# Optimization experiments

Hardware: AMD Instinct MI355X
Metric: run time of the kernel (lower is better)

## Reference

```python
import jax, jax.numpy as jnp
import numpy as np

HIDDEN = 128
N_NODES = 50000
N_NEI = 32


def setup_inputs() -> dict:
    key = jax.random.key(0)
    k1, k2, k3, k4, k5, k6 = jax.random.split(key, 6)
    x = jax.random.normal(k1, (N_NODES, HIDDEN), dtype=jnp.float32)
    neibour = jax.random.normal(k2, (N_NODES, N_NEI, HIDDEN), dtype=jnp.float32)
    sub_graph = jax.random.normal(k3, (N_NODES, HIDDEN), dtype=jnp.float32)
    pmi = jax.random.normal(k4, (N_NODES, N_NEI), dtype=jnp.float32)
    nei_pad_mask = jnp.zeros((N_NODES, N_NEI), dtype=jnp.float32)
    # nn.Linear(2H, 1): store weight as [2H, 1] plus bias [1]
    bound = 1.0 / np.sqrt(2 * HIDDEN)
    W = jax.random.uniform(k5, (2 * HIDDEN, 1), jnp.float32, -bound, bound)
    b = jax.random.uniform(k6, (1,), jnp.float32, -bound, bound)
    return {"x": x, "neibour": neibour, "sub_graph": sub_graph,
            "pmi": pmi, "nei_pad_mask": nei_pad_mask, "W": W, "b": b}


def reference(x, neibour, sub_graph, pmi, nei_pad_mask, W, b):
    # torch: cat([neibour, expand(sub_graph)], -1) @ W + b  (Linear(2H,1))
    # Split W so we never materialize the [N,K,2H] concat: same math.
    H = sub_graph.shape[-1]
    Wn, Ws = W[:H], W[H:]                                   # [H,1] each
    s = (jnp.einsum('nkh,ho->nko', neibour, Wn)             # [N,K,1]
         + jnp.einsum('nh,ho->no', sub_graph, Ws)[:, None, :]
         + b)
    score = jax.nn.sigmoid(s).sum(-1)                       # sum over singleton out dim -> [N,K]
    score = score + nei_pad_mask
    return jax.nn.softmax(score, axis=-1)
```

## Files before the change

### kernel.cpp

```cpp
#include <hip/hip_runtime.h>
#include <hip/hip_bf16.h>

#define HIDDEN 128
#define N_NEI 32

__device__ __forceinline__ float merge2(float a, float b, int m, int lane) {
    const bool hi = (lane & m) != 0;
    const float keep = hi ? b : a;
    const float send = hi ? a : b;
    return keep + __shfl_xor(send, m, 64);
}

__global__ __launch_bounds__(256) void score_softmax_kernel(
    const float* __restrict__ neibour,
    const float* __restrict__ sub_graph,
    const float* __restrict__ nei_pad_mask,
    const float* __restrict__ W,
    const float* __restrict__ b,
    float* __restrict__ out,
    int n_nodes)
{
    const int wave = threadIdx.x >> 6;
    const int lane = threadIdx.x & 63;
    const int node = blockIdx.x * 4 + wave;
    if (node >= n_nodes) return;

    const int half = lane >> 5;
    const int l32  = lane & 31;

    const float4 wn = *reinterpret_cast<const float4*>(W + l32 * 4);

    const float2 sg = *reinterpret_cast<const float2*>(sub_graph + (size_t)node * HIDDEN + lane * 2);
    const float2 ws = *reinterpret_cast<const float2*>(W + HIDDEN + lane * 2);
    float sn = fmaf(sg.x, ws.x, sg.y * ws.y);
    #pragma unroll
    for (int m = 1; m < 64; m <<= 1) sn += __shfl_xor(sn, m, 64);
    sn += b[0];

    const float* nb = neibour + (size_t)node * (N_NEI * HIDDEN);
    float p[16];
    #pragma unroll
    for (int kk = 0; kk < 16; ++kk) {
        const float4 v = *reinterpret_cast<const float4*>(nb + (2 * kk + half) * HIDDEN + l32 * 4);
        p[kk] = fmaf(v.x, wn.x, fmaf(v.y, wn.y, fmaf(v.z, wn.z, v.w * wn.w)));
    }

    float r[8];
    #pragma unroll
    for (int i = 0; i < 8; ++i) r[i] = merge2(p[2*i], p[2*i+1], 16, lane);
    float s4[4];
    #pragma unroll
    for (int i = 0; i < 4; ++i) s4[i] = merge2(r[2*i], r[2*i+1], 8, lane);
    float t2[2];
    #pragma unroll
    for (int i = 0; i < 2; ++i) t2[i] = merge2(s4[2*i], s4[2*i+1], 4, lane);
    float u = merge2(t2[0], t2[1], 2, lane);
    u += __shfl_xor(u, 1, 64);

    const int pidx = ((lane >> 4) & 1) | (((lane >> 3) & 1) << 1)
                   | (((lane >> 2) & 1) << 2) | (((lane >> 1) & 1) << 3);
    const int row = 2 * pidx + half;

    float sc = u + sn;
    sc = 1.0f / (1.0f + __expf(-sc));
    sc += nei_pad_mask[(size_t)node * N_NEI + row];

    float mx = sc;
    #pragma unroll
    for (int m = 1; m < 64; m <<= 1) mx = fmaxf(mx, __shfl_xor(mx, m, 64));
    float e = __expf(sc - mx);
    float ssum = e;
    #pragma unroll
    for (int m = 1; m < 64; m <<= 1) ssum += __shfl_xor(ssum, m, 64);

    if ((lane & 1) == 0)
        out[(size_t)node * N_NEI + row] = e * 2.0f / ssum;
}

extern "C" void kernel_launch(void* const* d_in, const int* in_sizes, int n_in,
                              void* d_out, int out_size, void* d_ws, size_t ws_size,
                              hipStream_t stream) {
    const float* neibour      = (const float*)d_in[1];
    const float* sub_graph    = (const float*)d_in[2];
    const float* nei_pad_mask = (const float*)d_in[4];
    const float* W            = (const float*)d_in[5];
    const float* b            = (const float*)d_in[6];
    float* out = (float*)d_out;

    const int n_nodes = in_sizes[4] / N_NEI;
    const int blocks  = (n_nodes + 3) / 4;

    score_softmax_kernel<<<blocks, 256, 0, stream>>>(
        neibour, sub_graph, nei_pad_mask, W, b, out, n_nodes);
}
```

Baseline: 148.9 us.

## Use persistent grid-stride waves with register prefetch of the next node

Launches a fixed grid of 1024 blocks in which each wave loops over nodes with a grid stride. The next node's neighbour rows, sub_graph slice and mask are loaded into registers before the current node's reductions and softmax run, so memory latency overlaps with compute. Loads and stores use nontemporal hints, and the max/sum reductions skip the redundant xor-1 step because lane pairs already hold duplicate values. The cost is roughly double the vector register use for the prefetch buffer, which may cut occupancy, and fewer waves in flight overall.

```diff
diff --git a/kernel.cpp b/kernel.cpp
--- a/kernel.cpp
+++ b/kernel.cpp
@@ -3,6 +3,8 @@
 
 #define HIDDEN 128
 #define N_NEI 32
+
+typedef float f32x4 __attribute__((ext_vector_type(4)));
 
 __device__ __forceinline__ float merge2(float a, float b, int m, int lane) {
     const bool hi = (lane & m) != 0;
@@ -22,59 +24,87 @@
 {
     const int wave = threadIdx.x >> 6;
     const int lane = threadIdx.x & 63;
-    const int node = blockIdx.x * 4 + wave;
-    if (node >= n_nodes) return;
-
     const int half = lane >> 5;
     const int l32  = lane & 31;
-
-    const float4 wn = *reinterpret_cast<const float4*>(W + l32 * 4);
-
-    const float2 sg = *reinterpret_cast<const float2*>(sub_graph + (size_t)node * HIDDEN + lane * 2);
-    const float2 ws = *reinterpret_cast<const float2*>(W + HIDDEN + lane * 2);
-    float sn = fmaf(sg.x, ws.x, sg.y * ws.y);
-    #pragma unroll
-    for (int m = 1; m < 64; m <<= 1) sn += __shfl_xor(sn, m, 64);
-    sn += b[0];
-
-    const float* nb = neibour + (size_t)node * (N_NEI * HIDDEN);
-    float p[16];
-    #pragma unroll
-    for (int kk = 0; kk < 16; ++kk) {
-        const float4 v = *reinterpret_cast<const float4*>(nb + (2 * kk + half) * HIDDEN + l32 * 4);
-        p[kk] = fmaf(v.x, wn.x, fmaf(v.y, wn.y, fmaf(v.z, wn.z, v.w * wn.w)));
-    }
-
-    float r[8];
-    #pragma unroll
-    for (int i = 0; i < 8; ++i) r[i] = merge2(p[2*i], p[2*i+1], 16, lane);
-    float s4[4];
-    #pragma unroll
-    for (int i = 0; i < 4; ++i) s4[i] = merge2(r[2*i], r[2*i+1], 8, lane);
-    float t2[2];
-    #pragma unroll
-    for (int i = 0; i < 2; ++i) t2[i] = merge2(s4[2*i], s4[2*i+1], 4, lane);
-    float u = merge2(t2[0], t2[1], 2, lane);
-    u += __shfl_xor(u, 1, 64);
+    const int wgid = blockIdx.x * 4 + wave;
+    const int wstride = gridDim.x * 4;
 
     const int pidx = ((lane >> 4) & 1) | (((lane >> 3) & 1) << 1)
                    | (((lane >> 2) & 1) << 2) | (((lane >> 1) & 1) << 3);
     const int row = 2 * pidx + half;
 
-    float sc = u + sn;
-    sc = 1.0f / (1.0f + __expf(-sc));
-    sc += nei_pad_mask[(size_t)node * N_NEI + row];
+    const f32x4 wn = *reinterpret_cast<const f32x4*>(W + l32 * 4);
+    const float2 ws = *reinterpret_cast<const float2*>(W + HIDDEN + lane * 2);
+    const float bias = b[0];
 
-    float mx = sc;
-    #pragma unroll
-    for (int m = 1; m < 64; m <<= 1) mx = fmaxf(mx, __shfl_xor(mx, m, 64));
-    float e = __expf(sc - mx);
-    float ssum = e;
-    #pragma unroll
-    for (int m = 1; m < 64; m <<= 1) ssum += __shfl_xor(ssum, m, 64);
+    int node = wgid;
+    if (node >= n_nodes) return;
 
-    if ((lane & 1) == 0)
-        out[(size_t)node * N_NEI + row] = e * 2.0f / ssum;
+    f32x4 v[16];
+    float2 sgv;
+    float maskv;
+
+#define LOAD_NODE(nd) do {                                                    \
+        const float* nb_ = neibour + (size_t)(nd) * (N_NEI * HIDDEN);         \
+        _Pragma("unroll")                                                     \
+        for (int kk = 0; kk < 16; ++kk)                                       \
+            v[kk] = __builtin_nontemporal_load(                               \
+                reinterpret_cast<const f32x4*>(nb_ + (2 * kk + half) * HIDDEN \
+                                               + l32 * 4));                   \
+        sgv = *reinterpret_cast<const float2*>(                               \
+            sub_graph + (size_t)(nd) * HIDDEN + lane * 2);                    \
+        maskv = nei_pad_mask[(size_t)(nd) * N_NEI + row];                     \
+    } while (0)
+
+    LOAD_NODE(node);
+
+    #pragma unroll 1
+    while (node < n_nodes) {
+        float p[16];
+        #pragma unroll
+        for (int kk = 0; kk < 16; ++kk)
+            p[kk] = fmaf(v[kk].x, wn.x, fmaf(v[kk].y, wn.y,
+                     fmaf(v[kk].z, wn.z, v[kk].w * wn.w)));
+        float sn = fmaf(sgv.x, ws.x, sgv.y * ws.y);
+        const float mask_cur = maskv;
+
+        const int next = node + wstride;
+        if (next < n_nodes) LOAD_NODE(next);
+
+        #pragma unroll
+        for (int m = 1; m < 64; m <<= 1) sn += __shfl_xor(sn, m, 64);
+        sn += bias;
+
+        float r[8];
+        #pragma unroll
+        for (int i = 0; i < 8; ++i) r[i] = merge2(p[2*i], p[2*i+1], 16, lane);
+        float s4[4];
+        #pragma unroll
+        for (int i = 0; i < 4; ++i) s4[i] = merge2(r[2*i], r[2*i+1], 8, lane);
+        float t2[2];
+        #pragma unroll
+        for (int i = 0; i < 2; ++i) t2[i] = merge2(s4[2*i], s4[2*i+1], 4, lane);
+        float u = merge2(t2[0], t2[1], 2, lane);
+        u += __shfl_xor(u, 1, 64);
+
+        float sc = u + sn;
+        sc = 1.0f / (1.0f + __expf(-sc));
+        sc += mask_cur;
+
+        float mx = sc;
+        #pragma unroll
+        for (int m = 2; m < 64; m <<= 1) mx = fmaxf(mx, __shfl_xor(mx, m, 64));
+        float e = __expf(sc - mx);
+        float ssum = e;
+        #pragma unroll
+        for (int m = 2; m < 64; m <<= 1) ssum += __shfl_xor(ssum, m, 64);
+
+        if ((lane & 1) == 0)
+            __builtin_nontemporal_store(e / ssum, out + (size_t)node * N_NEI + row);
+
+        node = next;
+    }
+#undef LOAD_NODE
 }
 
 extern "C" void kernel_launch(void* const* d_in, const int* in_sizes, int n_in,
@@ -88,7 +118,10 @@
     float* out = (float*)d_out;
 
     const int n_nodes = in_sizes[4] / N_NEI;
-    const int blocks  = (n_nodes + 3) / 4;
+
+    int blocks = 1024;
+    const int max_blocks = (n_nodes + 3) / 4;
+    if (blocks > max_blocks) blocks = max_blocks;
 
     score_softmax_kernel<<<blocks, 256, 0, stream>>>(
         neibour, sub_graph, nei_pad_mask, W, b, out, n_nodes);
```

New measurement: 140.2 us. 5.8% less time.
